# Kernel optimization log

Hardware: AMD Instinct MI355X
Metric: run time of the kernel (lower is better)

## Reference

```python
import jax, jax.numpy as jnp
import numpy as np

NUM_LAYER = 4
EMB = 64
ATOM_VOCAB = 64
BOND_VOCAB = 8
BN_EPS = 1e-5


def _batchnorm(h, gamma, beta):
    m = h.mean(axis=0)
    v = h.var(axis=0)
    return gamma * (h - m) * jax.lax.rsqrt(v + BN_EPS) + beta


def setup_inputs() -> dict:
    key = jax.random.key(0)
    ks = jax.random.split(key, 16)
    N, E, L = 100000, 1000000, NUM_LAYER
    x = jax.random.randint(ks[0], (N, 9), 0, ATOM_VOCAB)
    edge_index = jax.random.randint(ks[1], (2, E), 0, N)
    edge_attr = jax.random.randint(ks[2], (E, 3), 0, BOND_VOCAB)
    batch = jnp.sort(jax.random.randint(ks[3], (N,), 0, 512))
    s = 0.02
    atom_emb = jax.random.normal(ks[4], (9, ATOM_VOCAB, EMB), jnp.float32) * s
    bond_emb = jax.random.normal(ks[5], (L, 3, BOND_VOCAB, EMB), jnp.float32) * s
    eps = jnp.zeros((L,), jnp.float32)
    W1 = jax.random.normal(ks[6], (L, EMB, 2 * EMB), jnp.float32) * s
    b1 = jnp.zeros((L, 2 * EMB), jnp.float32)
    bn1_g = jnp.ones((L, 2 * EMB), jnp.float32)
    bn1_b = jnp.zeros((L, 2 * EMB), jnp.float32)
    W2 = jax.random.normal(ks[7], (L, 2 * EMB, EMB), jnp.float32) * s
    b2 = jnp.zeros((L, EMB), jnp.float32)
    bn_g = jnp.ones((L, EMB), jnp.float32)
    bn_b = jnp.zeros((L, EMB), jnp.float32)
    return dict(x=x, edge_index=edge_index, edge_attr=edge_attr, batch=batch,
                atom_emb=atom_emb, bond_emb=bond_emb, eps=eps,
                W1=W1, b1=b1, bn1_g=bn1_g, bn1_b=bn1_b,
                W2=W2, b2=b2, bn_g=bn_g, bn_b=bn_b)


def reference(x, edge_index, edge_attr, batch, atom_emb, bond_emb, eps,
              W1, b1, bn1_g, bn1_b, W2, b2, bn_g, bn_b):
    N = x.shape[0]
    src, dst = edge_index[0], edge_index[1]
    # AtomEncoder: sum embeddings over the 9 atom-feature columns
    h = sum(atom_emb[c][x[:, c]] for c in range(9))  # [N, EMB]
    for layer in range(NUM_LAYER):
        # BondEncoder for this layer
        ee = sum(bond_emb[layer, c][edge_attr[:, c]] for c in range(3))  # [E, EMB]
        # message: relu(x_j + edge_emb); aggregate: scatter-add at dst
        msg = jax.nn.relu(h[src] + ee)
        agg = jax.ops.segment_sum(msg, dst, num_segments=N)
        z = (1.0 + eps[layer]) * h + agg
        # MLP: Linear -> BN -> ReLU -> Linear
        z = z @ W1[layer] + b1[layer]
        z = jax.nn.relu(_batchnorm(z, bn1_g[layer], bn1_b[layer]))
        z = z @ W2[layer] + b2[layer]
        # outer BatchNorm, then ReLU on all but last layer (dropout = identity)
        z = _batchnorm(z, bn_g[layer], bn_b[layer])
        if layer < NUM_LAYER - 1:
            z = jax.nn.relu(z)
        h = z
    return (h, batch)
```

## Files before the change

kernel.cpp:

```cpp
#include <hip/hip_runtime.h>
#include <hip/hip_bf16.h>

#define N_NODES 100000
#define N_EDGES 1000000
#define EMB 64
#define NLAYER 4
#define NTILE 1563
#define NSB 391
#define NSHARD 16
#define NBIN 196
#define NS1B 489

typedef __hip_bfloat16 bf16;
typedef __attribute__((ext_vector_type(8))) short short8;
typedef __attribute__((ext_vector_type(4))) float f32x4;

static __device__ __forceinline__ float b2f(bf16 v) { return __bfloat162float(v); }
static __device__ __forceinline__ bf16 f2b(float v) { return __float2bfloat16(v); }

__global__ void k_atom(const int* __restrict__ x, const bf16* __restrict__ aemb,
                       bf16* __restrict__ P) {
    int tid = blockIdx.x * 256 + threadIdx.x;
    int n = tid >> 6, e = tid & 63;
    float s = 0.f;
#pragma unroll
    for (int c = 0; c < 9; ++c) {
        int v = x[n * 9 + c];
        s += b2f(aemb[(c * 64 + v) * 64 + e]);
    }
    P[tid] = f2b(s);
}

__global__ void k_bond(const bf16* __restrict__ bemb, bf16* __restrict__ cb) {
    int idx = blockIdx.x * 256 + threadIdx.x;
    int l = idx >> 15, r = idx & 32767;
    int combo = r >> 6, c = r & 63;
    int e0 = combo & 7, e1 = (combo >> 3) & 7, e2 = combo >> 6;
    float v = b2f(bemb[((l * 3 + 0) * 8 + e0) * 64 + c]) +
              b2f(bemb[((l * 3 + 1) * 8 + e1) * 64 + c]) +
              b2f(bemb[((l * 3 + 2) * 8 + e2) * 64 + c]);
    cb[idx] = f2b(v);
}

__global__ __launch_bounds__(1024) void k_hist(const int* __restrict__ ei,
                                               int* __restrict__ deg,
                                               int* __restrict__ bcnt) {
    __shared__ int lb[NBIN];
    for (int i = threadIdx.x; i < NBIN; i += 1024) lb[i] = 0;
    __syncthreads();
    int e = blockIdx.x * 1024 + threadIdx.x;
    if (e < N_EDGES) {
        int d = ei[N_EDGES + e];
        atomicAdd(&deg[d], 1);
        atomicAdd(&lb[d >> 9], 1);
    }
    __syncthreads();
    for (int i = threadIdx.x; i < NBIN; i += 1024)
        if (lb[i]) atomicAdd(&bcnt[i], lb[i]);
}

__global__ void k_scanA(const int* __restrict__ deg, int* __restrict__ bsum) {
    __shared__ int red[256];
    int i = blockIdx.x * 256 + threadIdx.x;
    red[threadIdx.x] = (i < N_NODES) ? deg[i] : 0;
    __syncthreads();
    for (int d = 128; d > 0; d >>= 1) {
        if (threadIdx.x < d) red[threadIdx.x] += red[threadIdx.x + d];
        __syncthreads();
    }
    if (threadIdx.x == 0) bsum[blockIdx.x] = red[0];
}

__global__ void k_scanB(const int* __restrict__ bsum, int* __restrict__ boff,
                        int* __restrict__ offs, const int* __restrict__ bcnt,
                        int* __restrict__ bbase, int* __restrict__ bcur) {
    __shared__ int s[512], s2[512];
    int t = threadIdx.x;
    int v0 = (t < NSB) ? bsum[t] : 0;
    int b0 = (t < NBIN) ? bcnt[t] : 0;
    s[t] = v0; s2[t] = b0;
    __syncthreads();
    for (int d = 1; d < 512; d <<= 1) {
        int va = (t >= d) ? s[t - d] : 0;
        int vb = (t >= d) ? s2[t - d] : 0;
        __syncthreads();
        s[t] += va; s2[t] += vb;
        __syncthreads();
    }
    if (t < NSB) boff[t] = s[t] - v0;
    if (t == 0) offs[N_NODES] = s[NSB - 1];
    if (t < NBIN) { int st = s2[t] - b0; bbase[t] = st; bcur[t] = st; }
}

__global__ void k_scanC(const int* __restrict__ deg, const int* __restrict__ boff,
                        int* __restrict__ offs, int* __restrict__ cursor) {
    __shared__ int s[256];
    int i = blockIdx.x * 256 + threadIdx.x;
    int t = threadIdx.x;
    int d0 = (i < N_NODES) ? deg[i] : 0;
    s[t] = d0;
    __syncthreads();
    for (int d = 1; d < 256; d <<= 1) {
        int v = (t >= d) ? s[t - d] : 0;
        __syncthreads();
        s[t] += v;
        __syncthreads();
    }
    if (i < N_NODES) {
        int off = boff[blockIdx.x] + s[t] - d0;
        offs[i] = off;
        cursor[i] = off;
    }
}

__global__ __launch_bounds__(256) void k_scat1(const int* __restrict__ ei,
                                               const int* __restrict__ ea,
                                               int* __restrict__ bcur,
                                               int2* __restrict__ tmp8,
                                               int* __restrict__ tmpd) {
    __shared__ int lcnt[NBIN], gb[NBIN], lcur[NBIN];
    for (int i = threadIdx.x; i < NBIN; i += 256) lcnt[i] = 0;
    __syncthreads();
    int base = blockIdx.x * 2048;
#pragma unroll
    for (int k = 0; k < 8; ++k) {
        int e = base + k * 256 + threadIdx.x;
        if (e < N_EDGES) atomicAdd(&lcnt[ei[N_EDGES + e] >> 9], 1);
    }
    __syncthreads();
    for (int i = threadIdx.x; i < NBIN; i += 256) {
        lcur[i] = 0;
        if (lcnt[i]) gb[i] = atomicAdd(&bcur[i], lcnt[i]);
    }
    __syncthreads();
#pragma unroll
    for (int k = 0; k < 8; ++k) {
        int e = base + k * 256 + threadIdx.x;
        if (e < N_EDGES) {
            int d = ei[N_EDGES + e];
            int bin = d >> 9;
            int pk = ea[e * 3] + (ea[e * 3 + 1] << 3) + (ea[e * 3 + 2] << 6);
            int r = atomicAdd(&lcur[bin], 1);
            int pos = gb[bin] + r;
            tmp8[pos] = make_int2(ei[e], pk);
            tmpd[pos] = d;
        }
    }
}

__global__ __launch_bounds__(256) void k_scat2(const int2* __restrict__ tmp8,
                                               const int* __restrict__ tmpd,
                                               const int* __restrict__ bbase,
                                               const int* __restrict__ bcur,
                                               int* __restrict__ cursor,
                                               int2* __restrict__ csr) {
    int bin = blockIdx.x;
    int s0 = bbase[bin], s1 = bcur[bin];
    for (int i = s0 + threadIdx.x; i < s1; i += 256) {
        int d = tmpd[i];
        int pos = atomicAdd(&cursor[d], 1);
        csr[pos] = tmp8[i];
    }
}

__global__ void k_agg(const bf16* __restrict__ P, const int* __restrict__ offs,
                      const int2* __restrict__ csr,
                      const bf16* __restrict__ cb, const bf16* __restrict__ eps,
                      const float* __restrict__ p2s, const bf16* __restrict__ g2,
                      const bf16* __restrict__ bb2, int layer,
                      bf16* __restrict__ G, float* __restrict__ p1s) {
    if (blockIdx.x < NSHARD) p1s[blockIdx.x * 256 + threadIdx.x] = 0.f;
    int tid = blockIdx.x * 256 + threadIdx.x;
    int c = tid & 63;
    int n = __builtin_amdgcn_readfirstlane(tid >> 6);
    float av = 1.f, cv = 0.f, lo = -3.4e38f;
    if (layer > 0) {
        const float* pp = p2s + (layer - 1) * NSHARD * 128;
        float S = 0.f, Q = 0.f;
#pragma unroll
        for (int s = 0; s < NSHARD; ++s) { S += pp[s * 128 + c]; Q += pp[s * 128 + 64 + c]; }
        float mean = S / (float)N_NODES;
        float var = fmaxf(Q / (float)N_NODES - mean * mean, 0.f);
        av = b2f(g2[(layer - 1) * 64 + c]) * rsqrtf(var + 1e-5f);
        cv = b2f(bb2[(layer - 1) * 64 + c]) - mean * av;
        lo = 0.f;
    }
    const bf16* cbl = cb + layer * 512 * 64;
    float hself = fmaxf(av * b2f(P[(size_t)n * 64 + c]) + cv, lo);
    float acc = (1.f + b2f(eps[layer])) * hself;
    int s0 = __builtin_amdgcn_readfirstlane(offs[n]);
    int s1 = __builtin_amdgcn_readfirstlane(offs[n + 1]);
    int i = s0;
    for (; i + 8 <= s1; i += 8) {
        int sr[8], ep[8];
        float hv[8], bv[8];
#pragma unroll
        for (int u = 0; u < 8; ++u) {
            int2 ed = csr[i + u];
            sr[u] = __builtin_amdgcn_readfirstlane(ed.x);
            ep[u] = __builtin_amdgcn_readfirstlane(ed.y);
        }
#pragma unroll
        for (int u = 0; u < 8; ++u) hv[u] = b2f(P[(size_t)sr[u] * 64 + c]);
#pragma unroll
        for (int u = 0; u < 8; ++u) bv[u] = b2f(cbl[(size_t)ep[u] * 64 + c]);
#pragma unroll
        for (int u = 0; u < 8; ++u)
            acc += fmaxf(fmaxf(av * hv[u] + cv, lo) + bv[u], 0.f);
    }
    for (; i + 4 <= s1; i += 4) {
        int sr[4], ep[4];
        float hv[4], bv[4];
#pragma unroll
        for (int u = 0; u < 4; ++u) {
            int2 ed = csr[i + u];
            sr[u] = __builtin_amdgcn_readfirstlane(ed.x);
            ep[u] = __builtin_amdgcn_readfirstlane(ed.y);
        }
#pragma unroll
        for (int u = 0; u < 4; ++u) hv[u] = b2f(P[(size_t)sr[u] * 64 + c]);
#pragma unroll
        for (int u = 0; u < 4; ++u) bv[u] = b2f(cbl[(size_t)ep[u] * 64 + c]);
#pragma unroll
        for (int u = 0; u < 4; ++u)
            acc += fmaxf(fmaxf(av * hv[u] + cv, lo) + bv[u], 0.f);
    }
    for (; i < s1; ++i) {
        int2 ed = csr[i];
        int sr = __builtin_amdgcn_readfirstlane(ed.x);
        int ep = __builtin_amdgcn_readfirstlane(ed.y);
        float m = fmaxf(av * b2f(P[(size_t)sr * 64 + c]) + cv, lo) +
                  b2f(cbl[(size_t)ep * 64 + c]);
        acc += fmaxf(m, 0.f);
    }
    G[tid] = f2b(acc);
}

__global__ void k_wt(const bf16* __restrict__ W1, const bf16* __restrict__ W2,
                     bf16* __restrict__ W1T, bf16* __restrict__ W2T) {
    int idx = blockIdx.x * 256 + threadIdx.x;
    int l = idx >> 13, r = idx & 8191;
    int k = r >> 7, n = r & 127;
    W1T[l * 8192 + n * 64 + k] = W1[idx];
    int k2 = r >> 6, n2 = r & 63;
    W2T[l * 8192 + n2 * 128 + k2] = W2[idx];
}

__global__ __launch_bounds__(256) void k_mlp1s(
    const bf16* __restrict__ X, const bf16* __restrict__ W1T, const bf16* __restrict__ b1,
    int layer, float* __restrict__ p1s, float* __restrict__ p2s) {
    __shared__ bf16 zt[64 * 72];
    __shared__ float ps[4][4][32];
    __shared__ float qs[4][4][32];
    if (blockIdx.x < NSHARD && threadIdx.x < 128)
        p2s[(layer * NSHARD + blockIdx.x) * 128 + threadIdx.x] = 0.f;
    const bf16* Wl = W1T + layer * 8192;
    int r0 = blockIdx.x * 64;
    int nrows = min(64, N_NODES - r0);
    for (int i = threadIdx.x; i < 512; i += 256) {
        int r = i >> 3, c = (i & 7) * 8;
        short8 v = {};
        if (r < nrows) v = *(const short8*)&X[(r0 + r) * 64 + c];
        *(short8*)&zt[r * 72 + c] = v;
    }
    __syncthreads();
    int wid = threadIdx.x >> 6;
    int l = threadIdx.x & 63;
    int l15 = l & 15, lq = l >> 4;
    f32x4 acc[4][2];
#pragma unroll
    for (int m = 0; m < 4; ++m)
#pragma unroll
        for (int n = 0; n < 2; ++n) acc[m][n] = (f32x4){0.f, 0.f, 0.f, 0.f};
#pragma unroll
    for (int s = 0; s < 2; ++s) {
        short8 a[4], b[2];
#pragma unroll
        for (int m = 0; m < 4; ++m)
            a[m] = *(const short8*)&zt[(m * 16 + l15) * 72 + s * 32 + lq * 8];
#pragma unroll
        for (int n = 0; n < 2; ++n)
            b[n] = *(const short8*)&Wl[(wid * 32 + n * 16 + l15) * 64 + s * 32 + lq * 8];
#pragma unroll
        for (int m = 0; m < 4; ++m)
#pragma unroll
            for (int n = 0; n < 2; ++n)
                acc[m][n] = __builtin_amdgcn_mfma_f32_16x16x32_bf16(a[m], b[n], acc[m][n], 0, 0, 0);
    }
    float bb[2], cs[2] = {0.f, 0.f}, cq[2] = {0.f, 0.f};
#pragma unroll
    for (int n = 0; n < 2; ++n) bb[n] = b2f(b1[layer * 128 + wid * 32 + n * 16 + l15]);
#pragma unroll
    for (int m = 0; m < 4; ++m)
#pragma unroll
        for (int r = 0; r < 4; ++r) {
            int row = m * 16 + lq * 4 + r;
            if (row < nrows) {
#pragma unroll
                for (int n = 0; n < 2; ++n) {
                    float v = acc[m][n][r] + bb[n];
                    cs[n] += v; cq[n] += v * v;
                }
            }
        }
#pragma unroll
    for (int n = 0; n < 2; ++n) {
        ps[wid][lq][n * 16 + l15] = cs[n];
        qs[wid][lq][n * 16 + l15] = cq[n];
    }
    __syncthreads();
    if (threadIdx.x < 128) {
        int t = threadIdx.x, ww = t >> 5, cc = t & 31;
        float S = 0.f, Q = 0.f;
#pragma unroll
        for (int s4 = 0; s4 < 4; ++s4) { S += ps[ww][s4][cc]; Q += qs[ww][s4][cc]; }
        int sh = blockIdx.x & (NSHARD - 1);
        atomicAdd(&p1s[sh * 256 + t], S);
        atomicAdd(&p1s[sh * 256 + 128 + t], Q);
    }
}

__global__ __launch_bounds__(256) void k_mlp2(
    const bf16* __restrict__ W1T, const bf16* __restrict__ b1,
    const bf16* __restrict__ g1, const bf16* __restrict__ bb1,
    const float* __restrict__ p1s,
    const bf16* __restrict__ W2T, const bf16* __restrict__ bias2, int layer,
    const bf16* __restrict__ X, bf16* __restrict__ Y, float* __restrict__ p2s) {
    __shared__ bf16 zt[64 * 72];
    __shared__ bf16 yt[64 * 136];
    __shared__ float ps2[4][4][16];
    __shared__ float qs2[4][4][16];
    const bf16* W1l = W1T + layer * 8192;
    const bf16* W2l = W2T + layer * 8192;
    int r0 = blockIdx.x * 64;
    int nrows = min(64, N_NODES - r0);
    for (int i = threadIdx.x; i < 512; i += 256) {
        int r = i >> 3, c = (i & 7) * 8;
        short8 v = {};
        if (r < nrows) v = *(const short8*)&X[(r0 + r) * 64 + c];
        *(short8*)&zt[r * 72 + c] = v;
    }
    __syncthreads();
    int wid = threadIdx.x >> 6;
    int l = threadIdx.x & 63;
    int l15 = l & 15, lq = l >> 4;
    {
        f32x4 acc[4][2];
#pragma unroll
        for (int m = 0; m < 4; ++m)
#pragma unroll
            for (int n = 0; n < 2; ++n) acc[m][n] = (f32x4){0.f, 0.f, 0.f, 0.f};
#pragma unroll
        for (int s = 0; s < 2; ++s) {
            short8 a[4], b[2];
#pragma unroll
            for (int m = 0; m < 4; ++m)
                a[m] = *(const short8*)&zt[(m * 16 + l15) * 72 + s * 32 + lq * 8];
#pragma unroll
            for (int n = 0; n < 2; ++n)
                b[n] = *(const short8*)&W1l[(wid * 32 + n * 16 + l15) * 64 + s * 32 + lq * 8];
#pragma unroll
            for (int m = 0; m < 4; ++m)
#pragma unroll
                for (int n = 0; n < 2; ++n)
                    acc[m][n] = __builtin_amdgcn_mfma_f32_16x16x32_bf16(a[m], b[n], acc[m][n], 0, 0, 0);
        }
        float aav[2], ccv[2], bbv[2];
#pragma unroll
        for (int n = 0; n < 2; ++n) {
            int col = wid * 32 + n * 16 + l15;
            float S = 0.f, Q = 0.f;
#pragma unroll
            for (int s4 = 0; s4 < NSHARD; ++s4) {
                S += p1s[s4 * 256 + col];
                Q += p1s[s4 * 256 + 128 + col];
            }
            float mean = S / (float)N_NODES;
            float var = fmaxf(Q / (float)N_NODES - mean * mean, 0.f);
            aav[n] = b2f(g1[layer * 128 + col]) * rsqrtf(var + 1e-5f);
            ccv[n] = b2f(bb1[layer * 128 + col]) - mean * aav[n];
            bbv[n] = b2f(b1[layer * 128 + col]);
        }
#pragma unroll
        for (int m = 0; m < 4; ++m)
#pragma unroll
            for (int n = 0; n < 2; ++n)
#pragma unroll
                for (int r = 0; r < 4; ++r) {
                    int row = m * 16 + lq * 4 + r;
                    float v = fmaxf(aav[n] * (acc[m][n][r] + bbv[n]) + ccv[n], 0.f);
                    yt[row * 136 + wid * 32 + n * 16 + l15] = f2b(v);
                }
    }
    __syncthreads();
    {
        f32x4 acc2[4];
#pragma unroll
        for (int m = 0; m < 4; ++m) acc2[m] = (f32x4){0.f, 0.f, 0.f, 0.f};
#pragma unroll
        for (int s = 0; s < 4; ++s) {
            short8 a[4];
            short8 b = *(const short8*)&W2l[(wid * 16 + l15) * 128 + s * 32 + lq * 8];
#pragma unroll
            for (int m = 0; m < 4; ++m)
                a[m] = *(const short8*)&yt[(m * 16 + l15) * 136 + s * 32 + lq * 8];
#pragma unroll
            for (int m = 0; m < 4; ++m)
                acc2[m] = __builtin_amdgcn_mfma_f32_16x16x32_bf16(a[m], b, acc2[m], 0, 0, 0);
        }
        float bb2 = b2f(bias2[layer * 64 + wid * 16 + l15]);
        float cs = 0.f, cq = 0.f;
#pragma unroll
        for (int m = 0; m < 4; ++m)
#pragma unroll
            for (int r = 0; r < 4; ++r) {
                int row = m * 16 + lq * 4 + r;
                float v = acc2[m][r] + bb2;
                zt[row * 72 + wid * 16 + l15] = f2b(v);
                if (row < nrows) { cs += v; cq += v * v; }
            }
        ps2[wid][lq][l15] = cs;
        qs2[wid][lq][l15] = cq;
    }
    __syncthreads();
    for (int i = threadIdx.x; i < 512; i += 256) {
        int r = i >> 3, c = (i & 7) * 8;
        if (r < nrows)
            *(short8*)&Y[(r0 + r) * 64 + c] = *(const short8*)&zt[r * 72 + c];
    }
    if (threadIdx.x < 64) {
        int ww = threadIdx.x >> 4, cc = threadIdx.x & 15;
        float S = 0.f, Q = 0.f;
#pragma unroll
        for (int s4 = 0; s4 < 4; ++s4) { S += ps2[ww][s4][cc]; Q += qs2[ww][s4][cc]; }
        int sh = blockIdx.x & (NSHARD - 1);
        atomicAdd(&p2s[(layer * NSHARD + sh) * 128 + threadIdx.x], S);
        atomicAdd(&p2s[(layer * NSHARD + sh) * 128 + 64 + threadIdx.x], Q);
    }
}

__global__ void k_out(const bf16* __restrict__ P, const float* __restrict__ p2s,
                      const bf16* __restrict__ g2, const bf16* __restrict__ bb2,
                      const int* __restrict__ batch, float* __restrict__ out) {
    int tid = blockIdx.x * 256 + threadIdx.x;
    int c = tid & 63;
    const float* pp = p2s + 3 * NSHARD * 128;
    float S = 0.f, Q = 0.f;
#pragma unroll
    for (int s = 0; s < NSHARD; ++s) { S += pp[s * 128 + c]; Q += pp[s * 128 + 64 + c]; }
    float mean = S / (float)N_NODES;
    float var = fmaxf(Q / (float)N_NODES - mean * mean, 0.f);
    float av = b2f(g2[3 * 64 + c]) * rsqrtf(var + 1e-5f);
    float cv = b2f(bb2[3 * 64 + c]) - mean * av;
    float v = b2f(f2b(av * b2f(P[tid]) + cv));
    out[tid] = (v != v || fabsf(v) > 1e20f) ? 0.f : v;
    if (tid < N_NODES) out[N_NODES * EMB + tid] = (float)batch[tid];
}

extern "C" void kernel_launch(void* const* d_in, const int* in_sizes, int n_in,
                              void* d_out, int out_size, void* d_ws, size_t ws_size,
                              hipStream_t stream) {
    (void)in_sizes; (void)n_in; (void)out_size; (void)ws_size;
    const int* x     = (const int*)d_in[0];
    const int* ei    = (const int*)d_in[1];
    const int* ea    = (const int*)d_in[2];
    const int* batch = (const int*)d_in[3];
    const bf16* aemb = (const bf16*)d_in[4];
    const bf16* bemb = (const bf16*)d_in[5];
    const bf16* eps  = (const bf16*)d_in[6];
    const bf16* W1   = (const bf16*)d_in[7];
    const bf16* b1   = (const bf16*)d_in[8];
    const bf16* g1   = (const bf16*)d_in[9];
    const bf16* bb1  = (const bf16*)d_in[10];
    const bf16* W2   = (const bf16*)d_in[11];
    const bf16* b2   = (const bf16*)d_in[12];
    const bf16* g2   = (const bf16*)d_in[13];
    const bf16* bb2  = (const bf16*)d_in[14];

    bf16* Y = (bf16*)d_ws;
    char* ob = (char*)d_out;
    bf16* X       = (bf16*)ob;
    int2* tmp8    = (int2*)ob;
    int*  tmpd    = (int*)(ob + 8000000);
    int*  deg     = (int*)(ob + 12800000);
    int*  offs    = (int*)(ob + 13200000);
    int*  cursor  = (int*)(ob + 13600008);
    int2* csr     = (int2*)(ob + 14000008);
    float* p1s    = (float*)(ob + 22000008);
    float* p2s    = (float*)(ob + 22016392);
    int*  bsum    = (int*)(ob + 22049160);
    int*  boff    = (int*)(ob + 22050724);
    bf16* w1t     = (bf16*)(ob + 22052288);
    bf16* w2t     = (bf16*)(ob + 22117824);
    bf16* cbt     = (bf16*)(ob + 22183360);
    int*  bcnt    = (int*)(ob + 22445504);
    int*  bbase   = (int*)(ob + 22446288);
    int*  bcur    = (int*)(ob + 22447072);

    hipMemsetAsync(deg, 0, 400000, stream);
    hipMemsetAsync(bcnt, 0, NBIN * 4, stream);

    k_atom<<<25000, 256, 0, stream>>>(x, aemb, Y);
    k_wt<<<128, 256, 0, stream>>>(W1, W2, w1t, w2t);
    k_bond<<<512, 256, 0, stream>>>(bemb, cbt);
    k_hist<<<977, 1024, 0, stream>>>(ei, deg, bcnt);
    k_scanA<<<NSB, 256, 0, stream>>>(deg, bsum);
    k_scanB<<<1, 512, 0, stream>>>(bsum, boff, offs, bcnt, bbase, bcur);
    k_scanC<<<NSB, 256, 0, stream>>>(deg, boff, offs, cursor);
    k_scat1<<<NS1B, 256, 0, stream>>>(ei, ea, bcur, tmp8, tmpd);
    k_scat2<<<NBIN, 256, 0, stream>>>(tmp8, tmpd, bbase, bcur, cursor, csr);

    for (int l = 0; l < NLAYER; ++l) {
        k_agg<<<25000, 256, 0, stream>>>(Y, offs, csr, cbt, eps,
                                         p2s, g2, bb2, l, X, p1s);
        k_mlp1s<<<NTILE, 256, 0, stream>>>(X, w1t, b1, l, p1s, p2s);
        k_mlp2<<<NTILE, 256, 0, stream>>>(w1t, b1, g1, bb1, p1s, w2t, b2, l, X, Y, p2s);
    }
    k_out<<<25000, 256, 0, stream>>>(Y, p2s, g2, bb2, batch, (float*)d_out);
}
```

Baseline: 586.1 us.

## Build CSR via deterministic per-block bin partials and in-LDS per-bin degree scan

Replaces the global per-node degree histogram, three-stage node scan, and global cursor atomics with a two-pass binned counting sort. Per-block bin counts are prefix-scanned per bin so scat1 no longer needs global atomics. Each scat2 block then computes node degrees and offsets for its 512-node bin in LDS. This removes two memsets, several kernels and a million global atomics, in exchange for an extra pass over the edge bins in scat2.

```diff
diff --git a/kernel.cpp b/kernel.cpp
--- a/kernel.cpp
+++ b/kernel.cpp
@@ -6,7 +6,6 @@
 #define EMB 64
 #define NLAYER 4
 #define NTILE 1563
-#define NSB 391
 #define NSHARD 16
 #define NBIN 196
 #define NS1B 489
@@ -42,63 +41,45 @@
     cb[idx] = f2b(v);
 }
 
-__global__ __launch_bounds__(1024) void k_hist(const int* __restrict__ ei,
-                                               int* __restrict__ deg,
+
+__global__ __launch_bounds__(256) void k_binc(const int* __restrict__ ei,
+                                              int* __restrict__ bpart) {
+    __shared__ int lc[NBIN];
+    for (int i = threadIdx.x; i < NBIN; i += 256) lc[i] = 0;
+    __syncthreads();
+    int base = blockIdx.x * 2048;
+#pragma unroll
+    for (int k = 0; k < 8; ++k) {
+        int e = base + k * 256 + threadIdx.x;
+        if (e < N_EDGES) atomicAdd(&lc[ei[N_EDGES + e] >> 9], 1);
+    }
+    __syncthreads();
+    for (int i = threadIdx.x; i < NBIN; i += 256) bpart[blockIdx.x * NBIN + i] = lc[i];
+}
+
+__global__ __launch_bounds__(512) void k_binps(int* __restrict__ bpart,
                                                int* __restrict__ bcnt) {
-    __shared__ int lb[NBIN];
-    for (int i = threadIdx.x; i < NBIN; i += 1024) lb[i] = 0;
-    __syncthreads();
-    int e = blockIdx.x * 1024 + threadIdx.x;
-    if (e < N_EDGES) {
-        int d = ei[N_EDGES + e];
-        atomicAdd(&deg[d], 1);
-        atomicAdd(&lb[d >> 9], 1);
-    }
-    __syncthreads();
-    for (int i = threadIdx.x; i < NBIN; i += 1024)
-        if (lb[i]) atomicAdd(&bcnt[i], lb[i]);
-}
-
-__global__ void k_scanA(const int* __restrict__ deg, int* __restrict__ bsum) {
-    __shared__ int red[256];
-    int i = blockIdx.x * 256 + threadIdx.x;
-    red[threadIdx.x] = (i < N_NODES) ? deg[i] : 0;
-    __syncthreads();
-    for (int d = 128; d > 0; d >>= 1) {
-        if (threadIdx.x < d) red[threadIdx.x] += red[threadIdx.x + d];
+    __shared__ int s[512];
+    int bin = blockIdx.x, t = threadIdx.x;
+    int v0 = (t < NS1B) ? bpart[t * NBIN + bin] : 0;
+    s[t] = v0;
+    __syncthreads();
+    for (int d = 1; d < 512; d <<= 1) {
+        int v = (t >= d) ? s[t - d] : 0;
         __syncthreads();
-    }
-    if (threadIdx.x == 0) bsum[blockIdx.x] = red[0];
-}
-
-__global__ void k_scanB(const int* __restrict__ bsum, int* __restrict__ boff,
-                        int* __restrict__ offs, const int* __restrict__ bcnt,
-                        int* __restrict__ bbase, int* __restrict__ bcur) {
-    __shared__ int s[512], s2[512];
+        s[t] += v;
+        __syncthreads();
+    }
+    if (t < NS1B) bpart[t * NBIN + bin] = s[t] - v0;
+    if (t == 511) bcnt[bin] = s[511];
+}
+
+__global__ void k_binbase(const int* __restrict__ bcnt, int* __restrict__ bbase,
+                          int* __restrict__ offs) {
+    __shared__ int s[256];
     int t = threadIdx.x;
-    int v0 = (t < NSB) ? bsum[t] : 0;
-    int b0 = (t < NBIN) ? bcnt[t] : 0;
-    s[t] = v0; s2[t] = b0;
-    __syncthreads();
-    for (int d = 1; d < 512; d <<= 1) {
-        int va = (t >= d) ? s[t - d] : 0;
-        int vb = (t >= d) ? s2[t - d] : 0;
-        __syncthreads();
-        s[t] += va; s2[t] += vb;
-        __syncthreads();
-    }
-    if (t < NSB) boff[t] = s[t] - v0;
-    if (t == 0) offs[N_NODES] = s[NSB - 1];
-    if (t < NBIN) { int st = s2[t] - b0; bbase[t] = st; bcur[t] = st; }
-}
-
-__global__ void k_scanC(const int* __restrict__ deg, const int* __restrict__ boff,
-                        int* __restrict__ offs, int* __restrict__ cursor) {
-    __shared__ int s[256];
-    int i = blockIdx.x * 256 + threadIdx.x;
-    int t = threadIdx.x;
-    int d0 = (i < N_NODES) ? deg[i] : 0;
-    s[t] = d0;
+    int v0 = (t < NBIN) ? bcnt[t] : 0;
+    s[t] = v0;
     __syncthreads();
     for (int d = 1; d < 256; d <<= 1) {
         int v = (t >= d) ? s[t - d] : 0;
@@ -106,33 +87,23 @@
         s[t] += v;
         __syncthreads();
     }
-    if (i < N_NODES) {
-        int off = boff[blockIdx.x] + s[t] - d0;
-        offs[i] = off;
-        cursor[i] = off;
-    }
+    if (t < NBIN) bbase[t] = s[t] - v0;
+    if (t == 0) offs[N_NODES] = N_EDGES;
 }
 
 __global__ __launch_bounds__(256) void k_scat1(const int* __restrict__ ei,
                                                const int* __restrict__ ea,
-                                               int* __restrict__ bcur,
+                                               const int* __restrict__ bpart,
+                                               const int* __restrict__ bbase,
                                                int2* __restrict__ tmp8,
                                                int* __restrict__ tmpd) {
-    __shared__ int lcnt[NBIN], gb[NBIN], lcur[NBIN];
-    for (int i = threadIdx.x; i < NBIN; i += 256) lcnt[i] = 0;
+    __shared__ int gb[NBIN], lcur[NBIN];
+    for (int i = threadIdx.x; i < NBIN; i += 256) {
+        gb[i] = bbase[i] + bpart[blockIdx.x * NBIN + i];
+        lcur[i] = 0;
+    }
     __syncthreads();
     int base = blockIdx.x * 2048;
-#pragma unroll
-    for (int k = 0; k < 8; ++k) {
-        int e = base + k * 256 + threadIdx.x;
-        if (e < N_EDGES) atomicAdd(&lcnt[ei[N_EDGES + e] >> 9], 1);
-    }
-    __syncthreads();
-    for (int i = threadIdx.x; i < NBIN; i += 256) {
-        lcur[i] = 0;
-        if (lcnt[i]) gb[i] = atomicAdd(&bcur[i], lcnt[i]);
-    }
-    __syncthreads();
 #pragma unroll
     for (int k = 0; k < 8; ++k) {
         int e = base + k * 256 + threadIdx.x;
@@ -148,17 +119,37 @@
     }
 }
 
-__global__ __launch_bounds__(256) void k_scat2(const int2* __restrict__ tmp8,
+__global__ __launch_bounds__(512) void k_scat2(const int2* __restrict__ tmp8,
                                                const int* __restrict__ tmpd,
                                                const int* __restrict__ bbase,
-                                               const int* __restrict__ bcur,
-                                               int* __restrict__ cursor,
+                                               const int* __restrict__ bcnt,
+                                               int* __restrict__ offs,
                                                int2* __restrict__ csr) {
-    int bin = blockIdx.x;
-    int s0 = bbase[bin], s1 = bcur[bin];
-    for (int i = s0 + threadIdx.x; i < s1; i += 256) {
+    __shared__ int dg[512], sc[512], cur[512];
+    int bin = blockIdx.x, t = threadIdx.x;
+    dg[t] = 0;
+    __syncthreads();
+    int s0 = bbase[bin], cnt = bcnt[bin];
+    for (int i = s0 + t; i < s0 + cnt; i += 512)
+        atomicAdd(&dg[tmpd[i] & 511], 1);
+    __syncthreads();
+    int v0 = dg[t];
+    sc[t] = v0;
+    __syncthreads();
+    for (int d = 1; d < 512; d <<= 1) {
+        int v = (t >= d) ? sc[t - d] : 0;
+        __syncthreads();
+        sc[t] += v;
+        __syncthreads();
+    }
+    int ex = s0 + sc[t] - v0;
+    cur[t] = ex;
+    int node = (bin << 9) + t;
+    if (node < N_NODES) offs[node] = ex;
+    __syncthreads();
+    for (int i = s0 + t; i < s0 + cnt; i += 512) {
         int d = tmpd[i];
-        int pos = atomicAdd(&cursor[d], 1);
+        int pos = atomicAdd(&cur[d & 511], 1);
         csr[pos] = tmp8[i];
     }
 }
@@ -482,33 +473,25 @@
     bf16* X       = (bf16*)ob;
     int2* tmp8    = (int2*)ob;
     int*  tmpd    = (int*)(ob + 8000000);
-    int*  deg     = (int*)(ob + 12800000);
     int*  offs    = (int*)(ob + 13200000);
-    int*  cursor  = (int*)(ob + 13600008);
     int2* csr     = (int2*)(ob + 14000008);
     float* p1s    = (float*)(ob + 22000008);
     float* p2s    = (float*)(ob + 22016392);
-    int*  bsum    = (int*)(ob + 22049160);
-    int*  boff    = (int*)(ob + 22050724);
-    bf16* w1t     = (bf16*)(ob + 22052288);
-    bf16* w2t     = (bf16*)(ob + 22117824);
-    bf16* cbt     = (bf16*)(ob + 22183360);
-    int*  bcnt    = (int*)(ob + 22445504);
-    int*  bbase   = (int*)(ob + 22446288);
-    int*  bcur    = (int*)(ob + 22447072);
-
-    hipMemsetAsync(deg, 0, 400000, stream);
-    hipMemsetAsync(bcnt, 0, NBIN * 4, stream);
+    int*  bpart   = (int*)(ob + 22049160);
+    int*  bcnt    = (int*)(ob + 22432536);
+    int*  bbase   = (int*)(ob + 22433320);
+    bf16* w1t     = (bf16*)(ob + 22434112);
+    bf16* w2t     = (bf16*)(ob + 22499648);
+    bf16* cbt     = (bf16*)(ob + 22565184);
 
     k_atom<<<25000, 256, 0, stream>>>(x, aemb, Y);
     k_wt<<<128, 256, 0, stream>>>(W1, W2, w1t, w2t);
     k_bond<<<512, 256, 0, stream>>>(bemb, cbt);
-    k_hist<<<977, 1024, 0, stream>>>(ei, deg, bcnt);
-    k_scanA<<<NSB, 256, 0, stream>>>(deg, bsum);
-    k_scanB<<<1, 512, 0, stream>>>(bsum, boff, offs, bcnt, bbase, bcur);
-    k_scanC<<<NSB, 256, 0, stream>>>(deg, boff, offs, cursor);
-    k_scat1<<<NS1B, 256, 0, stream>>>(ei, ea, bcur, tmp8, tmpd);
-    k_scat2<<<NBIN, 256, 0, stream>>>(tmp8, tmpd, bbase, bcur, cursor, csr);
+    k_binc<<<NS1B, 256, 0, stream>>>(ei, bpart);
+    k_binps<<<NBIN, 512, 0, stream>>>(bpart, bcnt);
+    k_binbase<<<1, 256, 0, stream>>>(bcnt, bbase, offs);
+    k_scat1<<<NS1B, 256, 0, stream>>>(ei, ea, bpart, bbase, tmp8, tmpd);
+    k_scat2<<<NBIN, 512, 0, stream>>>(tmp8, tmpd, bbase, bcnt, offs, csr);
 
     for (int l = 0; l < NLAYER; ++l) {
         k_agg<<<25000, 256, 0, stream>>>(Y, offs, csr, cbt, eps,
```

Result: faster. 504.3 us (-14.0%).
